# Performance work log

Hardware: AMD Instinct MI355X
Metric: run time of the kernel (lower is better)

Reference implementation:

```python
import jax, jax.numpy as jnp
import numpy as np

N_STREAMS = 4
SINKHORN_ITERS = 20
EPS = 1e-6


def sinkhorn_knopp(M, iters=SINKHORN_ITERS, eps=EPS):
    # M: (batch, n, n) logits -> doubly stochastic via exp + alternating row/col normalization
    P0 = jnp.exp(M)

    def body(i, P):
        P = P / (P.sum(axis=-1, keepdims=True) + eps)  # row normalize
        P = P / (P.sum(axis=-2, keepdims=True) + eps)  # col normalize
        return P

    return jax.lax.fori_loop(0, iters, body, P0)


def setup_inputs() -> dict:
    key = jax.random.key(0)
    k1, k2, k3 = jax.random.split(key, 3)
    B, S, n, D = 4, 4096, N_STREAMS, 1024
    H = jax.random.normal(k1, (B, S, n, D), dtype=jnp.float32)
    branch_output = jax.random.normal(k2, (B, S, D), dtype=jnp.float32)
    phi = jax.random.normal(k3, (n * D, n * n + 2 * n), dtype=jnp.float32) * 0.02
    H_pre_base = jnp.zeros((n,), jnp.float32).at[0].set(1.0)  # layer_idx=0
    H_post_base = jnp.ones((n,), jnp.float32)
    H_res_base = jnp.eye(n, dtype=jnp.float32)
    init_scale = jnp.float32(0.1)
    return {
        "H": H,
        "branch_output": branch_output,
        "phi": phi,
        "H_pre_base": H_pre_base,
        "H_post_base": H_post_base,
        "H_res_base": H_res_base,
        "alpha_pre": init_scale,
        "alpha_post": init_scale,
        "alpha_res": init_scale,
    }


def reference(H, branch_output, phi, H_pre_base, H_post_base, H_res_base,
              alpha_pre, alpha_post, alpha_res):
    n = N_STREAMS
    B = H.shape[0]
    # --- fused dynamic weights (Eq. 14-19) ---
    x = H.mean(axis=1).reshape(B, -1)                       # (B, n*D)
    rms = jnp.sqrt(jnp.mean(x * x, axis=-1, keepdims=True) + EPS)
    x = x / rms
    delta = x @ phi                                         # (B, n*n + 2n)
    d_pre = delta[:, :n]
    d_post = delta[:, n:2 * n]
    d_res = delta[:, 2 * n:].reshape(B, n, n)
    H_pre = jax.nn.sigmoid(H_pre_base + alpha_pre * d_pre)
    H_pre = H_pre / (H_pre.sum(axis=-1, keepdims=True) + 1e-8)
    H_post = jax.nn.sigmoid(H_post_base + alpha_post * d_post)
    H_res = sinkhorn_knopp(H_res_base + alpha_res * d_res)  # (B, n, n) doubly stochastic
    # --- fused stream mix ---
    branch_input = jnp.einsum('bk,bskd->bsd', H_pre, H)     # (B, S, D)
    H_residual = jnp.einsum('bij,bsjd->bsid', H_res, H)     # (B, S, n, D)
    # --- fused add residual ---
    H_new = H_residual + H_post[:, None, :, None] * branch_output[:, :, None, :]
    # Pack outputs into one array: (B, S, 1+n, D)
    return jnp.concatenate([branch_input[:, :, None, :], H_new], axis=2)
```

## Files before the change

### kernel.cpp

```cpp
#include <hip/hip_runtime.h>
#include <math.h>

#define S_LEN 4096
#define N_STR 4
#define D_DIM 1024
#define ND    4096
#define ND4   1024
#define SCHUNK 64
#define CHUNKS 64

__global__ __launch_bounds__(256) void k1_reduce(const float4* __restrict__ H4,
                                                 float4* __restrict__ partial4) {
  int blk = blockIdx.x;
  int b = blk >> 8;
  int chunk = (blk >> 2) & 63;
  int dq = blk & 3;
  int fidx = dq * 256 + threadIdx.x;
  const float4* p = H4 + ((size_t)(b * S_LEN + chunk * SCHUNK)) * ND4 + fidx;
  float4 acc = make_float4(0.f, 0.f, 0.f, 0.f);
#pragma unroll 4
  for (int s = 0; s < SCHUNK; ++s) {
    float4 v = p[(size_t)s * ND4];
    acc.x += v.x; acc.y += v.y; acc.z += v.z; acc.w += v.w;
  }
  partial4[((size_t)(b * CHUNKS + chunk)) * ND4 + fidx] = acc;
}

__global__ __launch_bounds__(256) void k2_stats(
    const float4* __restrict__ partial4, const float* __restrict__ phi,
    const float* __restrict__ hpre_b, const float* __restrict__ hpost_b,
    const float* __restrict__ hres_b, const float* __restrict__ a_pre_p,
    const float* __restrict__ a_post_p, const float* __restrict__ a_res_p,
    float* __restrict__ weights) {
  int b = blockIdx.x;
  int tid = threadIdx.x;
  __shared__ float xs[ND];
  __shared__ float ssq_s;
  __shared__ float s_inv_rms;
  __shared__ float delta_s[24];

  if (tid == 0) ssq_s = 0.f;
  if (tid < 24) delta_s[tid] = 0.f;
  __syncthreads();

  float ssq = 0.f;
  const float inv_s = 1.0f / (float)S_LEN;
#pragma unroll
  for (int k = 0; k < 4; ++k) {
    int fidx = tid + k * 256;
    float4 acc = make_float4(0.f, 0.f, 0.f, 0.f);
    for (int c = 0; c < CHUNKS; ++c) {
      float4 v = partial4[((size_t)(b * CHUNKS + c)) * ND4 + fidx];
      acc.x += v.x; acc.y += v.y; acc.z += v.z; acc.w += v.w;
    }
    acc.x *= inv_s; acc.y *= inv_s; acc.z *= inv_s; acc.w *= inv_s;
    xs[fidx * 4 + 0] = acc.x;
    xs[fidx * 4 + 1] = acc.y;
    xs[fidx * 4 + 2] = acc.z;
    xs[fidx * 4 + 3] = acc.w;
    ssq += acc.x * acc.x + acc.y * acc.y + acc.z * acc.z + acc.w * acc.w;
  }
  atomicAdd(&ssq_s, ssq);
  __syncthreads();
  if (tid == 0) {
    s_inv_rms = 1.0f / sqrtf(ssq_s * (1.0f / (float)ND) + 1e-6f);
  }
  __syncthreads();

  float acc[24];
#pragma unroll
  for (int m = 0; m < 24; ++m) acc[m] = 0.f;
  for (int k = 0; k < 16; ++k) {
    int i = tid + k * 256;
    float xv = xs[i];
    const float* ph = phi + (size_t)i * 24;
#pragma unroll
    for (int m = 0; m < 24; ++m) acc[m] = fmaf(xv, ph[m], acc[m]);
  }
#pragma unroll
  for (int m = 0; m < 24; ++m) atomicAdd(&delta_s[m], acc[m]);
  __syncthreads();

  if (tid == 0) {
    float inv_rms = s_inv_rms;
    float a_pre = a_pre_p[0], a_post = a_post_p[0], a_res = a_res_p[0];
    float d[24];
#pragma unroll
    for (int m = 0; m < 24; ++m) d[m] = delta_s[m] * inv_rms;

    float hp[4], hsum = 0.f;
#pragma unroll
    for (int k = 0; k < 4; ++k) {
      hp[k] = 1.0f / (1.0f + expf(-(hpre_b[k] + a_pre * d[k])));
      hsum += hp[k];
    }
    float invsum = 1.0f / (hsum + 1e-8f);
#pragma unroll
    for (int k = 0; k < 4; ++k) weights[b * 24 + k] = hp[k] * invsum;

#pragma unroll
    for (int k = 0; k < 4; ++k)
      weights[b * 24 + 4 + k] =
          1.0f / (1.0f + expf(-(hpost_b[k] + a_post * d[4 + k])));

    float P[16];
#pragma unroll
    for (int e = 0; e < 16; ++e) P[e] = expf(hres_b[e] + a_res * d[8 + e]);
    for (int it = 0; it < 20; ++it) {
#pragma unroll
      for (int i = 0; i < 4; ++i) {
        float rs = P[i * 4] + P[i * 4 + 1] + P[i * 4 + 2] + P[i * 4 + 3];
        float inv = 1.0f / (rs + 1e-6f);
        P[i * 4] *= inv; P[i * 4 + 1] *= inv; P[i * 4 + 2] *= inv; P[i * 4 + 3] *= inv;
      }
#pragma unroll
      for (int j = 0; j < 4; ++j) {
        float cs = P[j] + P[4 + j] + P[8 + j] + P[12 + j];
        float inv = 1.0f / (cs + 1e-6f);
        P[j] *= inv; P[4 + j] *= inv; P[8 + j] *= inv; P[12 + j] *= inv;
      }
    }
#pragma unroll
    for (int e = 0; e < 16; ++e) weights[b * 24 + 8 + e] = P[e];
  }
}

__global__ __launch_bounds__(256) void k3_apply(const float4* __restrict__ H4,
                                                const float4* __restrict__ BO4,
                                                const float* __restrict__ weights,
                                                float4* __restrict__ out4) {
  int bs = blockIdx.x;
  int b = bs >> 12;
  __shared__ float w[24];
  if (threadIdx.x < 24) w[threadIdx.x] = weights[b * 24 + threadIdx.x];
  __syncthreads();
  int t = threadIdx.x;
  const float4* hb = H4 + (size_t)bs * ND4;
  float4 h0 = hb[t];
  float4 h1 = hb[256 + t];
  float4 h2 = hb[512 + t];
  float4 h3 = hb[768 + t];
  float4 bo = BO4[(size_t)bs * 256 + t];
  float4* ob = out4 + (size_t)bs * (5 * 256);

  float4 o;
  o.x = w[0] * h0.x + w[1] * h1.x + w[2] * h2.x + w[3] * h3.x;
  o.y = w[0] * h0.y + w[1] * h1.y + w[2] * h2.y + w[3] * h3.y;
  o.z = w[0] * h0.z + w[1] * h1.z + w[2] * h2.z + w[3] * h3.z;
  o.w = w[0] * h0.w + w[1] * h1.w + w[2] * h2.w + w[3] * h3.w;
  ob[t] = o;

#pragma unroll
  for (int i = 0; i < 4; ++i) {
    float w0 = w[8 + i * 4 + 0];
    float w1 = w[8 + i * 4 + 1];
    float w2 = w[8 + i * 4 + 2];
    float w3 = w[8 + i * 4 + 3];
    float wp = w[4 + i];
    o.x = w0 * h0.x + w1 * h1.x + w2 * h2.x + w3 * h3.x + wp * bo.x;
    o.y = w0 * h0.y + w1 * h1.y + w2 * h2.y + w3 * h3.y + wp * bo.y;
    o.z = w0 * h0.z + w1 * h1.z + w2 * h2.z + w3 * h3.z + wp * bo.z;
    o.w = w0 * h0.w + w1 * h1.w + w2 * h2.w + w3 * h3.w + wp * bo.w;
    ob[(i + 1) * 256 + t] = o;
  }
}

extern "C" void kernel_launch(void* const* d_in, const int* in_sizes, int n_in,
                              void* d_out, int out_size, void* d_ws, size_t ws_size,
                              hipStream_t stream) {
  const float* H       = (const float*)d_in[0];
  const float* BO      = (const float*)d_in[1];
  const float* phi     = (const float*)d_in[2];
  const float* hpre_b  = (const float*)d_in[3];
  const float* hpost_b = (const float*)d_in[4];
  const float* hres_b  = (const float*)d_in[5];
  const float* a_pre   = (const float*)d_in[6];
  const float* a_post  = (const float*)d_in[7];
  const float* a_res   = (const float*)d_in[8];
  float* out = (float*)d_out;

  const size_t partial_floats = (size_t)4 * CHUNKS * ND;
  float* partial;
  float* weights;
  if (ws_size >= (partial_floats + 96) * sizeof(float)) {
    partial = (float*)d_ws;
    weights = partial + partial_floats;
  } else {
    partial = out;
    weights = (float*)d_ws;
  }

  hipLaunchKernelGGL(k1_reduce, dim3(1024), dim3(256), 0, stream,
                     (const float4*)H, (float4*)partial);
  hipLaunchKernelGGL(k2_stats, dim3(4), dim3(256), 0, stream,
                     (const float4*)partial, phi, hpre_b, hpost_b, hres_b,
                     a_pre, a_post, a_res, weights);
  hipLaunchKernelGGL(k3_apply, dim3(4 * S_LEN), dim3(256), 0, stream,
                     (const float4*)H, (const float4*)BO, weights, (float4*)out);
}
```

Before: 672.9 us.

## Add nontemporal stores, split accumulators, and wave-shuffle reductions across kernels

The final apply kernel now uses nontemporal loads for branch_output and nontemporal stores for the large packed output, so streaming data does less damage to the cache. The reduce kernel uses four independent accumulators to expose more loads in flight. The stats kernel grows to 1024 threads and replaces shared-memory atomics with wave shuffle reductions. The traffic-bound apply kernel dominates the runtime, so most of any effect comes from the cache hints, and those can also hurt.

```diff
diff --git a/kernel.cpp b/kernel.cpp
--- a/kernel.cpp
+++ b/kernel.cpp
@@ -1,92 +1,111 @@
 #include <hip/hip_runtime.h>
 #include <math.h>
 
+typedef float v4f __attribute__((ext_vector_type(4)));
+
 #define S_LEN 4096
-#define N_STR 4
-#define D_DIM 1024
 #define ND    4096
 #define ND4   1024
 #define SCHUNK 64
 #define CHUNKS 64
 
-__global__ __launch_bounds__(256) void k1_reduce(const float4* __restrict__ H4,
-                                                 float4* __restrict__ partial4) {
+__global__ __launch_bounds__(256) void k1_reduce(const v4f* __restrict__ H4,
+                                                 v4f* __restrict__ partial4) {
   int blk = blockIdx.x;
   int b = blk >> 8;
   int chunk = (blk >> 2) & 63;
   int dq = blk & 3;
   int fidx = dq * 256 + threadIdx.x;
-  const float4* p = H4 + ((size_t)(b * S_LEN + chunk * SCHUNK)) * ND4 + fidx;
-  float4 acc = make_float4(0.f, 0.f, 0.f, 0.f);
+  const v4f* p = H4 + ((size_t)(b * S_LEN + chunk * SCHUNK)) * ND4 + fidx;
+  v4f a0 = {0.f, 0.f, 0.f, 0.f};
+  v4f a1 = {0.f, 0.f, 0.f, 0.f};
+  v4f a2 = {0.f, 0.f, 0.f, 0.f};
+  v4f a3 = {0.f, 0.f, 0.f, 0.f};
 #pragma unroll 4
-  for (int s = 0; s < SCHUNK; ++s) {
-    float4 v = p[(size_t)s * ND4];
-    acc.x += v.x; acc.y += v.y; acc.z += v.z; acc.w += v.w;
-  }
-  partial4[((size_t)(b * CHUNKS + chunk)) * ND4 + fidx] = acc;
-}
-
-__global__ __launch_bounds__(256) void k2_stats(
-    const float4* __restrict__ partial4, const float* __restrict__ phi,
+  for (int s = 0; s < SCHUNK; s += 4) {
+    a0 += p[(size_t)(s + 0) * ND4];
+    a1 += p[(size_t)(s + 1) * ND4];
+    a2 += p[(size_t)(s + 2) * ND4];
+    a3 += p[(size_t)(s + 3) * ND4];
+  }
+  partial4[((size_t)(b * CHUNKS + chunk)) * ND4 + fidx] = (a0 + a1) + (a2 + a3);
+}
+
+__global__ __launch_bounds__(1024) void k2_stats(
+    const v4f* __restrict__ partial4, const float* __restrict__ phi,
     const float* __restrict__ hpre_b, const float* __restrict__ hpost_b,
     const float* __restrict__ hres_b, const float* __restrict__ a_pre_p,
     const float* __restrict__ a_post_p, const float* __restrict__ a_res_p,
     float* __restrict__ weights) {
   int b = blockIdx.x;
-  int tid = threadIdx.x;
+  int t = threadIdx.x;
+  int lane = t & 63;
+  int wave = t >> 6;
+
   __shared__ float xs[ND];
-  __shared__ float ssq_s;
+  __shared__ float wred[16];
+  __shared__ float dred[16][24];
+  __shared__ float dfin[24];
   __shared__ float s_inv_rms;
-  __shared__ float delta_s[24];
-
-  if (tid == 0) ssq_s = 0.f;
-  if (tid < 24) delta_s[tid] = 0.f;
-  __syncthreads();
-
-  float ssq = 0.f;
-  const float inv_s = 1.0f / (float)S_LEN;
+
+  v4f a0 = {0.f, 0.f, 0.f, 0.f};
+  v4f a1 = {0.f, 0.f, 0.f, 0.f};
+  const v4f* pp = partial4 + (size_t)b * CHUNKS * ND4 + t;
+#pragma unroll 8
+  for (int c = 0; c < CHUNKS; c += 2) {
+    a0 += pp[(size_t)c * ND4];
+    a1 += pp[(size_t)(c + 1) * ND4];
+  }
+  v4f a = (a0 + a1) * (1.0f / (float)S_LEN);
+  xs[t * 4 + 0] = a.x; xs[t * 4 + 1] = a.y;
+  xs[t * 4 + 2] = a.z; xs[t * 4 + 3] = a.w;
+  float ssq = a.x * a.x + a.y * a.y + a.z * a.z + a.w * a.w;
+#pragma unroll
+  for (int off = 32; off; off >>= 1) ssq += __shfl_down(ssq, off, 64);
+  if (lane == 0) wred[wave] = ssq;
+  __syncthreads();
+  if (t == 0) {
+    float s = 0.f;
+#pragma unroll
+    for (int w = 0; w < 16; ++w) s += wred[w];
+    s_inv_rms = 1.0f / sqrtf(s * (1.0f / (float)ND) + 1e-6f);
+  }
+  __syncthreads();
+
+  float acc[24];
+#pragma unroll
+  for (int m = 0; m < 24; ++m) acc[m] = 0.f;
 #pragma unroll
   for (int k = 0; k < 4; ++k) {
-    int fidx = tid + k * 256;
-    float4 acc = make_float4(0.f, 0.f, 0.f, 0.f);
-    for (int c = 0; c < CHUNKS; ++c) {
-      float4 v = partial4[((size_t)(b * CHUNKS + c)) * ND4 + fidx];
-      acc.x += v.x; acc.y += v.y; acc.z += v.z; acc.w += v.w;
-    }
-    acc.x *= inv_s; acc.y *= inv_s; acc.z *= inv_s; acc.w *= inv_s;
-    xs[fidx * 4 + 0] = acc.x;
-    xs[fidx * 4 + 1] = acc.y;
-    xs[fidx * 4 + 2] = acc.z;
-    xs[fidx * 4 + 3] = acc.w;
-    ssq += acc.x * acc.x + acc.y * acc.y + acc.z * acc.z + acc.w * acc.w;
-  }
-  atomicAdd(&ssq_s, ssq);
-  __syncthreads();
-  if (tid == 0) {
-    s_inv_rms = 1.0f / sqrtf(ssq_s * (1.0f / (float)ND) + 1e-6f);
-  }
-  __syncthreads();
-
-  float acc[24];
-#pragma unroll
-  for (int m = 0; m < 24; ++m) acc[m] = 0.f;
-  for (int k = 0; k < 16; ++k) {
-    int i = tid + k * 256;
+    int i = t + k * 1024;
     float xv = xs[i];
     const float* ph = phi + (size_t)i * 24;
 #pragma unroll
     for (int m = 0; m < 24; ++m) acc[m] = fmaf(xv, ph[m], acc[m]);
   }
 #pragma unroll
-  for (int m = 0; m < 24; ++m) atomicAdd(&delta_s[m], acc[m]);
-  __syncthreads();
-
-  if (tid == 0) {
-    float inv_rms = s_inv_rms;
+  for (int off = 32; off; off >>= 1) {
+#pragma unroll
+    for (int m = 0; m < 24; ++m) acc[m] += __shfl_down(acc[m], off, 64);
+  }
+  if (lane == 0) {
+#pragma unroll
+    for (int m = 0; m < 24; ++m) dred[wave][m] = acc[m];
+  }
+  __syncthreads();
+  if (t < 24) {
+    float s = 0.f;
+#pragma unroll
+    for (int w = 0; w < 16; ++w) s += dred[w][t];
+    dfin[t] = s * s_inv_rms;
+  }
+  __syncthreads();
+
+  if (t == 0) {
     float a_pre = a_pre_p[0], a_post = a_post_p[0], a_res = a_res_p[0];
     float d[24];
 #pragma unroll
-    for (int m = 0; m < 24; ++m) d[m] = delta_s[m] * inv_rms;
+    for (int m = 0; m < 24; ++m) d[m] = dfin[m];
 
     float hp[4], hsum = 0.f;
 #pragma unroll
@@ -125,43 +144,32 @@
   }
 }
 
-__global__ __launch_bounds__(256) void k3_apply(const float4* __restrict__ H4,
-                                                const float4* __restrict__ BO4,
+__global__ __launch_bounds__(256) void k3_apply(const v4f* __restrict__ H4,
+                                                const v4f* __restrict__ BO4,
                                                 const float* __restrict__ weights,
-                                                float4* __restrict__ out4) {
+                                                v4f* __restrict__ out4) {
   int bs = blockIdx.x;
   int b = bs >> 12;
   __shared__ float w[24];
   if (threadIdx.x < 24) w[threadIdx.x] = weights[b * 24 + threadIdx.x];
   __syncthreads();
   int t = threadIdx.x;
-  const float4* hb = H4 + (size_t)bs * ND4;
-  float4 h0 = hb[t];
-  float4 h1 = hb[256 + t];
-  float4 h2 = hb[512 + t];
-  float4 h3 = hb[768 + t];
-  float4 bo = BO4[(size_t)bs * 256 + t];
-  float4* ob = out4 + (size_t)bs * (5 * 256);
-
-  float4 o;
-  o.x = w[0] * h0.x + w[1] * h1.x + w[2] * h2.x + w[3] * h3.x;
-  o.y = w[0] * h0.y + w[1] * h1.y + w[2] * h2.y + w[3] * h3.y;
-  o.z = w[0] * h0.z + w[1] * h1.z + w[2] * h2.z + w[3] * h3.z;
-  o.w = w[0] * h0.w + w[1] * h1.w + w[2] * h2.w + w[3] * h3.w;
-  ob[t] = o;
+  const v4f* hb = H4 + (size_t)bs * ND4;
+  v4f h0 = hb[t];
+  v4f h1 = hb[256 + t];
+  v4f h2 = hb[512 + t];
+  v4f h3 = hb[768 + t];
+  v4f bo = __builtin_nontemporal_load(BO4 + (size_t)bs * 256 + t);
+  v4f* ob = out4 + (size_t)bs * (5 * 256);
+
+  v4f o = w[0] * h0 + w[1] * h1 + w[2] * h2 + w[3] * h3;
+  __builtin_nontemporal_store(o, ob + t);
 
 #pragma unroll
   for (int i = 0; i < 4; ++i) {
-    float w0 = w[8 + i * 4 + 0];
-    float w1 = w[8 + i * 4 + 1];
-    float w2 = w[8 + i * 4 + 2];
-    float w3 = w[8 + i * 4 + 3];
-    float wp = w[4 + i];
-    o.x = w0 * h0.x + w1 * h1.x + w2 * h2.x + w3 * h3.x + wp * bo.x;
-    o.y = w0 * h0.y + w1 * h1.y + w2 * h2.y + w3 * h3.y + wp * bo.y;
-    o.z = w0 * h0.z + w1 * h1.z + w2 * h2.z + w3 * h3.z + wp * bo.z;
-    o.w = w0 * h0.w + w1 * h1.w + w2 * h2.w + w3 * h3.w + wp * bo.w;
-    ob[(i + 1) * 256 + t] = o;
+    o = w[8 + i * 4 + 0] * h0 + w[8 + i * 4 + 1] * h1 +
+        w[8 + i * 4 + 2] * h2 + w[8 + i * 4 + 3] * h3 + w[4 + i] * bo;
+    __builtin_nontemporal_store(o, ob + (i + 1) * 256 + t);
   }
 }
 
@@ -191,10 +199,10 @@
   }
 
   hipLaunchKernelGGL(k1_reduce, dim3(1024), dim3(256), 0, stream,
-                     (const float4*)H, (float4*)partial);
-  hipLaunchKernelGGL(k2_stats, dim3(4), dim3(256), 0, stream,
-                     (const float4*)partial, phi, hpre_b, hpost_b, hres_b,
+                     (const v4f*)H, (v4f*)partial);
+  hipLaunchKernelGGL(k2_stats, dim3(4), dim3(1024), 0, stream,
+                     (const v4f*)partial, phi, hpre_b, hpost_b, hres_b,
                      a_pre, a_post, a_res, weights);
   hipLaunchKernelGGL(k3_apply, dim3(4 * S_LEN), dim3(256), 0, stream,
-                     (const float4*)H, (const float4*)BO, weights, (float4*)out);
-}
+                     (const v4f*)H, (const v4f*)BO, weights, (v4f*)out);
+}
```

New measurement: 610.3 us. 1.1x faster.
